# Kernel tuning notes

Measured on AMD Instinct MI355X. Metric: run time of the kernel, lower is better.

Reference implementation:

```python
import jax, jax.numpy as jnp
import numpy as np
from jax import lax

N, IN, OUT, R, K = 16384, 128, 128, 3, 16
H = IN  # DGL lstm aggregator: LSTM(in_feats, in_feats)


def setup_inputs() -> dict:
    key = jax.random.key(0)
    ks = jax.random.split(key, 10)
    s_in = np.float32(1.0 / np.sqrt(IN))
    return {
        "x": jax.random.normal(ks[0], (N, IN), jnp.float32),
        "conn": jax.random.normal(ks[1], (N, IN), jnp.float32),
        "nbr_idx": jax.random.randint(ks[2], (R, N, K), 0, N),
        "trans": jax.random.normal(ks[3], (OUT, IN), jnp.float32) * s_in,
        "W_ih": jax.random.normal(ks[4], (R, 4 * H, IN), jnp.float32) * s_in,
        "W_hh": jax.random.normal(ks[5], (R, 4 * H, H), jnp.float32) * s_in,
        "b_lstm": jnp.zeros((R, 4 * H), jnp.float32),
        "fc_self": jax.random.normal(ks[6], (R, OUT, IN), jnp.float32) * s_in,
        "fc_neigh": jax.random.normal(ks[7], (R, OUT, H), jnp.float32) * s_in,
        "bias": jnp.zeros((R, OUT), jnp.float32),
    }


def _lstm_last_hidden(seq, Wih, Whh, b):
    """seq: [N, K, IN] neighbor sequence -> final hidden state [N, H].
    PyTorch/DGL gate order: input, forget, cell, output."""
    n = seq.shape[0]
    h0 = jnp.zeros((n, H), seq.dtype)
    c0 = jnp.zeros((n, H), seq.dtype)

    def step(carry, x_t):
        h, c = carry
        gates = x_t @ Wih.T + h @ Whh.T + b  # [N, 4H]
        i, f, g, o = jnp.split(gates, 4, axis=-1)
        i = jax.nn.sigmoid(i)
        f = jax.nn.sigmoid(f)
        o = jax.nn.sigmoid(o)
        g = jnp.tanh(g)
        c = f * c + i * g
        h = o * jnp.tanh(c)
        return (h, c), None

    (h, _), _ = lax.scan(step, (h0, c0), jnp.swapaxes(seq, 0, 1))  # scan over K
    return h


def reference(x, conn, nbr_idx, trans, W_ih, W_hh, b_lstm, fc_self, fc_neigh, bias):
    outs = []
    for r in range(R):  # small fixed relation set
        nbr = x[nbr_idx[r]]  # [N, K, IN] irregular gather
        h_n = _lstm_last_hidden(nbr, W_ih[r], W_hh[r], b_lstm[r])
        o = x @ fc_self[r].T + h_n @ fc_neigh[r].T + bias[r]
        outs.append(jax.nn.leaky_relu(o))  # slope 0.01 == F.leaky_relu default
    X = jnp.stack(outs, axis=1)  # [N, R, OUT]
    # att_score = (X @ trans) @ conn[:, :, None], softmax over relations
    score = jnp.einsum('nrd,di,ni->nr', X, trans, conn)
    att = jax.nn.softmax(score, axis=1)
    return jnp.einsum('nrd,nr->nd', X, att)  # [N, OUT]
```

## Files before the change

kernel.cpp:

```cpp
#include <hip/hip_runtime.h>

#define NN    16384
#define HD    128
#define G4    512
#define KST   16
#define NRELS 3

using f16x8 = __attribute__((ext_vector_type(8))) _Float16;
using f32x4 = __attribute__((ext_vector_type(4))) float;

static __device__ __forceinline__ f32x4 f4splat(float v) {
    f32x4 r; r[0] = v; r[1] = v; r[2] = v; r[3] = v; return r;
}
static __device__ __forceinline__ f16x8 load8h(const float* p) {
    const float4 a = ((const float4*)p)[0];
    const float4 b = ((const float4*)p)[1];
    f16x8 r;
    r[0] = (_Float16)a.x; r[1] = (_Float16)a.y; r[2] = (_Float16)a.z; r[3] = (_Float16)a.w;
    r[4] = (_Float16)b.x; r[5] = (_Float16)b.y; r[6] = (_Float16)b.z; r[7] = (_Float16)b.w;
    return r;
}
static __device__ __forceinline__ f32x4 mfma16h(f16x8 a, f16x8 b, f32x4 c) {
    return __builtin_amdgcn_mfma_f32_16x16x32_f16(a, b, c, 0, 0, 0);
}
static __device__ __forceinline__ unsigned short f2h_bits(float f) {
    return __builtin_bit_cast(unsigned short, (_Float16)f);
}
static __device__ __forceinline__ float h2f(unsigned short b) {
    return (float)__builtin_bit_cast(_Float16, b);
}
static __device__ __forceinline__ float sigm(float x) {
    return __builtin_amdgcn_rcpf(1.0f + __expf(-x));
}
static __device__ __forceinline__ float tanh_(float x) {
    return 2.0f * __builtin_amdgcn_rcpf(1.0f + __expf(-2.0f * x)) - 1.0f;
}

template <int OUTC, int MODE>
__global__ __launch_bounds__(512, 2) void gemm_rt(
    const float* __restrict__ A, const float* __restrict__ W,
    const float* __restrict__ bias, void* __restrict__ outp)
{
    constexpr int CW = OUTC / 8;
    constexpr int CT = CW / 16;
    const int tid = threadIdx.x;
    const int w = tid >> 6, lane = tid & 63;
    const int g = lane >> 4, m = lane & 15;
    const int n0 = blockIdx.x * 64;
    const int r = blockIdx.y;
    const float* Wr = W + (size_t)r * OUTC * HD;

    f32x4 acc[4][CT];
#pragma unroll
    for (int rt = 0; rt < 4; ++rt)
#pragma unroll
        for (int ct = 0; ct < CT; ++ct) acc[rt][ct] = f4splat(0.0f);

#pragma unroll
    for (int kc = 0; kc < 4; ++kc) {
        f16x8 a[4];
#pragma unroll
        for (int rt = 0; rt < 4; ++rt)
            a[rt] = load8h(A + (size_t)(n0 + rt * 16 + m) * HD + kc * 32 + 8 * g);
        f16x8 b[CT];
#pragma unroll
        for (int ct = 0; ct < CT; ++ct)
            b[ct] = load8h(Wr + (size_t)(w * CW + ct * 16 + m) * HD + kc * 32 + 8 * g);
#pragma unroll
        for (int rt = 0; rt < 4; ++rt)
#pragma unroll
            for (int ct = 0; ct < CT; ++ct)
                acc[rt][ct] = mfma16h(a[rt], b[ct], acc[rt][ct]);
    }

#pragma unroll
    for (int rt = 0; rt < 4; ++rt)
#pragma unroll
        for (int ct = 0; ct < CT; ++ct) {
            const int col = w * CW + ct * 16 + m;
            const float bv = bias ? bias[r * OUTC + col] : 0.0f;
#pragma unroll
            for (int e = 0; e < 4; ++e) {
                const int row = n0 + rt * 16 + 4 * g + e;
                const float v = acc[rt][ct][e] + bv;
                if constexpr (MODE == 0) {
                    ((float*)outp)[(size_t)row * OUTC + col] = v;
                } else {
                    ((unsigned short*)outp)[((size_t)r * NN + row) * G4 + (size_t)(col & 127) * 4 + (col >> 7)] =
                        f2h_bits(v);
                }
            }
        }
}

__global__ __launch_bounds__(512, 2) void lstm_kernel(
    const float* __restrict__ x, const int* __restrict__ nbr,
    const float* __restrict__ Whh, const float* __restrict__ fcs,
    const float* __restrict__ fcn, const float* __restrict__ bias,
    const unsigned short* __restrict__ xW, float* __restrict__ Xout)
{
    __shared__ unsigned short h_lds[2][64 * HD];
    __shared__ int idx_lds[64 * KST];

    const int tid = threadIdx.x;
    const int w = tid >> 6, lane = tid & 63;
    const int g = lane >> 4, m = lane & 15;
    const int n0 = blockIdx.x * 64;
    const int r = blockIdx.y;

    for (int i = tid; i < 64 * KST; i += 512)
        idx_lds[i] = nbr[((size_t)r * NN + n0 + (i >> 4)) * KST + (i & 15)];

    f16x8 bw[4][4];
    const float* whr = Whh + (size_t)r * G4 * HD;
#pragma unroll
    for (int q = 0; q < 4; ++q)
#pragma unroll
        for (int kc = 0; kc < 4; ++kc)
            bw[q][kc] = load8h(whr + (size_t)(q * 128 + w * 16 + m) * HD + kc * 32 + 8 * g);

    float cst[4][4];
#pragma unroll
    for (int rt = 0; rt < 4; ++rt)
#pragma unroll
        for (int e = 0; e < 4; ++e) cst[rt][e] = 0.0f;

    const unsigned short* xwr = xW + (size_t)r * NN * G4;
    __syncthreads();

    ushort4 xv[4][4];
#pragma unroll
    for (int rt = 0; rt < 4; ++rt)
#pragma unroll
        for (int e = 0; e < 4; ++e) {
            const int nidx = idx_lds[(rt * 16 + 4 * g + e) * KST + 0];
            xv[rt][e] = *(const ushort4*)(xwr + (size_t)nidx * G4 + (size_t)(w * 16 + m) * 4);
        }

    int cur = 0;
    for (int t = 0; t < KST; ++t) {
        f32x4 acc[4][4];
#pragma unroll
        for (int rt = 0; rt < 4; ++rt)
#pragma unroll
            for (int e = 0; e < 4; ++e) {
                acc[rt][0][e] = h2f(xv[rt][e].x);
                acc[rt][1][e] = h2f(xv[rt][e].y);
                acc[rt][2][e] = h2f(xv[rt][e].z);
                acc[rt][3][e] = h2f(xv[rt][e].w);
            }

        if (t + 1 < KST) {
#pragma unroll
            for (int rt = 0; rt < 4; ++rt)
#pragma unroll
                for (int e = 0; e < 4; ++e) {
                    const int nidx = idx_lds[(rt * 16 + 4 * g + e) * KST + (t + 1)];
                    xv[rt][e] = *(const ushort4*)(xwr + (size_t)nidx * G4 + (size_t)(w * 16 + m) * 4);
                }
        }

        if (t > 0) {
            const unsigned short* hb = h_lds[cur];
#pragma unroll
            for (int kc = 0; kc < 4; ++kc) {
                f16x8 a[4];
#pragma unroll
                for (int rt = 0; rt < 4; ++rt) {
                    const int row = rt * 16 + m;
                    a[rt] = *(const f16x8*)&hb[row * HD + ((kc * 32 + 8 * g) ^ ((row & 7) << 3))];
                }
#pragma unroll
                for (int rt = 0; rt < 4; ++rt)
#pragma unroll
                    for (int q = 0; q < 4; ++q)
                        acc[rt][q] = mfma16h(a[rt], bw[q][kc], acc[rt][q]);
            }
        }

        unsigned short* nh = h_lds[cur ^ 1];
#pragma unroll
        for (int rt = 0; rt < 4; ++rt)
#pragma unroll
            for (int e = 0; e < 4; ++e) {
                const float iv = sigm(acc[rt][0][e]);
                const float fv = sigm(acc[rt][1][e]);
                const float gv = tanh_(acc[rt][2][e]);
                const float ov = sigm(acc[rt][3][e]);
                const float cn = fv * cst[rt][e] + iv * gv;
                cst[rt][e] = cn;
                const float hf = ov * tanh_(cn);
                const int row = rt * 16 + 4 * g + e;
                const int col = w * 16 + m;
                nh[row * HD + (col ^ ((row & 7) << 3))] = f2h_bits(hf);
            }
        __syncthreads();
        cur ^= 1;
    }

    {
        const int rt = w & 3;
        const int cth = (w >> 2) * 64;
        const float* fsr = fcs + (size_t)r * HD * HD;
        const float* fnr = fcn + (size_t)r * HD * HD;
        const unsigned short* hb = h_lds[cur];
        f32x4 oacc[4];
#pragma unroll
        for (int i = 0; i < 4; ++i)
            oacc[i] = f4splat(bias[r * HD + cth + i * 16 + m]);
#pragma unroll
        for (int kc = 0; kc < 4; ++kc) {
            const int row = rt * 16 + m;
            const f16x8 ax = load8h(x + (size_t)(n0 + row) * HD + kc * 32 + 8 * g);
            const f16x8 ah = *(const f16x8*)&hb[row * HD + ((kc * 32 + 8 * g) ^ ((row & 7) << 3))];
#pragma unroll
            for (int i = 0; i < 4; ++i) {
                const f16x8 bs = load8h(fsr + (size_t)(cth + i * 16 + m) * HD + kc * 32 + 8 * g);
                const f16x8 bn = load8h(fnr + (size_t)(cth + i * 16 + m) * HD + kc * 32 + 8 * g);
                oacc[i] = mfma16h(ax, bs, oacc[i]);
                oacc[i] = mfma16h(ah, bn, oacc[i]);
            }
        }
#pragma unroll
        for (int i = 0; i < 4; ++i)
#pragma unroll
            for (int e = 0; e < 4; ++e) {
                const int row = rt * 16 + 4 * g + e;
                const int col = cth + i * 16 + m;
                float v = oacc[i][e];
                v = v > 0.0f ? v : 0.01f * v;
                Xout[((size_t)(n0 + row) * NRELS + r) * HD + col] = v;
            }
    }
}

__global__ __launch_bounds__(256) void attn_kernel(
    const float* __restrict__ X, const float* __restrict__ tc,
    float* __restrict__ out)
{
    const int wv = blockIdx.x * (blockDim.x >> 6) + (threadIdx.x >> 6);
    const int lane = threadIdx.x & 63;
    if (wv >= NN) return;
    const size_t nb = (size_t)wv;

    const float t0 = tc[nb * HD + lane];
    const float t1 = tc[nb * HD + 64 + lane];
    float x0[3], x1[3], sc[3];
#pragma unroll
    for (int r = 0; r < 3; ++r) {
        x0[r] = X[(nb * 3 + r) * HD + lane];
        x1[r] = X[(nb * 3 + r) * HD + 64 + lane];
        float p = x0[r] * t0 + x1[r] * t1;
#pragma unroll
        for (int off = 32; off >= 1; off >>= 1)
            p += __shfl_xor(p, off, 64);
        sc[r] = p;
    }
    const float mx = fmaxf(sc[0], fmaxf(sc[1], sc[2]));
    const float e0 = __expf(sc[0] - mx), e1 = __expf(sc[1] - mx), e2 = __expf(sc[2] - mx);
    const float inv = __builtin_amdgcn_rcpf(e0 + e1 + e2);
    const float a0 = e0 * inv, a1 = e1 * inv, a2 = e2 * inv;
    out[nb * HD + lane]      = a0 * x0[0] + a1 * x0[1] + a2 * x0[2];
    out[nb * HD + 64 + lane] = a0 * x1[0] + a1 * x1[1] + a2 * x1[2];
}

extern "C" void kernel_launch(void* const* d_in, const int* in_sizes, int n_in,
                              void* d_out, int out_size, void* d_ws, size_t ws_size,
                              hipStream_t stream)
{
    const float* x     = (const float*)d_in[0];
    const float* conn  = (const float*)d_in[1];
    const int*   nbr   = (const int*)d_in[2];
    const float* trans = (const float*)d_in[3];
    const float* Wih   = (const float*)d_in[4];
    const float* Whh   = (const float*)d_in[5];
    const float* blstm = (const float*)d_in[6];
    const float* fcs   = (const float*)d_in[7];
    const float* fcn   = (const float*)d_in[8];
    const float* bias  = (const float*)d_in[9];
    float* out = (float*)d_out;

    const size_t XW_B = (size_t)NRELS * NN * G4 * 2;
    const size_t TC_B = (size_t)NN * HD * 4;
    const size_t XO_B = (size_t)NN * NRELS * HD * 4;
    if (ws_size < XW_B + TC_B + XO_B) return;

    char* wsb = (char*)d_ws;
    unsigned short* xW = (unsigned short*)wsb;
    float*          tc = (float*)(wsb + XW_B);
    float*          Xo = (float*)(wsb + XW_B + TC_B);

    gemm_rt<512, 1><<<dim3(NN / 64, NRELS), 512, 0, stream>>>(x, Wih, blstm, (void*)xW);
    gemm_rt<128, 0><<<dim3(NN / 64, 1), 512, 0, stream>>>(conn, trans, nullptr, (void*)tc);
    lstm_kernel<<<dim3(NN / 64, NRELS), 512, 0, stream>>>(x, nbr, Whh, fcs, fcn, bias, xW, Xo);
    attn_kernel<<<dim3(NN / 4), 256, 0, stream>>>(Xo, tc, out);
}
```

Baseline: 349.4 us.

## Split LSTM block into two half-tiles and interleave MFMA with gate math

Splits the 64-row tile of the recurrent LSTM loop into two independent 32-row halves (A and B), each with its own LDS hidden-state buffer and cell state. Each half-step runs the MFMA recurrence for one half while the other half does its sigmoid/tanh gate math, so matrix and transcendental work can overlap across the barrier. It also pre-scales neighbor indices into byte offsets in LDS so the gather address needs only one add. The cost is two barriers per timestep instead of one and more live registers, which matters under the 512-thread, 2-block launch bound.

```diff
diff --git a/kernel.cpp b/kernel.cpp
--- a/kernel.cpp
+++ b/kernel.cpp
@@ -93,13 +93,71 @@
         }
 }
 
+static __device__ __forceinline__ void consume_xw(f32x4 (&acc)[2][4], const ushort4 (&xv)[2][4]) {
+#pragma unroll
+    for (int rt = 0; rt < 2; ++rt)
+#pragma unroll
+        for (int e = 0; e < 4; ++e) {
+            acc[rt][0][e] = h2f(xv[rt][e].x);
+            acc[rt][1][e] = h2f(xv[rt][e].y);
+            acc[rt][2][e] = h2f(xv[rt][e].z);
+            acc[rt][3][e] = h2f(xv[rt][e].w);
+        }
+}
+static __device__ __forceinline__ void prefetch_xw(ushort4 (&xv)[2][4], const int* idxt, int t,
+                                                   const char* xwr, int laneoff, int g) {
+#pragma unroll
+    for (int rt = 0; rt < 2; ++rt)
+#pragma unroll
+        for (int e = 0; e < 4; ++e) {
+            const unsigned off = (unsigned)idxt[(rt * 16 + 4 * g + e) * KST + t] + laneoff;
+            xv[rt][e] = *(const ushort4*)(xwr + off);
+        }
+}
+static __device__ __forceinline__ void mfma_h(f32x4 (&acc)[2][4], const unsigned short* hbuf,
+                                              const f16x8 (&bw)[4][4], int m, int g) {
+#pragma unroll
+    for (int kc = 0; kc < 4; ++kc) {
+        f16x8 a[2];
+#pragma unroll
+        for (int rt = 0; rt < 2; ++rt) {
+            const int row = rt * 16 + m;
+            a[rt] = *(const f16x8*)&hbuf[row * HD + ((kc * 32 + 8 * g) ^ ((row & 7) << 3))];
+        }
+#pragma unroll
+        for (int rt = 0; rt < 2; ++rt)
+#pragma unroll
+            for (int q = 0; q < 4; ++q)
+                acc[rt][q] = mfma16h(a[rt], bw[q][kc], acc[rt][q]);
+    }
+}
+static __device__ __forceinline__ void lstm_elem(const f32x4 (&acc)[2][4], float (&cst)[2][4],
+                                                 unsigned short* hbuf, int g, int m, int w) {
+#pragma unroll
+    for (int rt = 0; rt < 2; ++rt)
+#pragma unroll
+        for (int e = 0; e < 4; ++e) {
+            const float iv = sigm(acc[rt][0][e]);
+            const float fv = sigm(acc[rt][1][e]);
+            const float gv = tanh_(acc[rt][2][e]);
+            const float ov = sigm(acc[rt][3][e]);
+            const float cn = fv * cst[rt][e] + iv * gv;
+            cst[rt][e] = cn;
+            const float hf = ov * tanh_(cn);
+            const int row = rt * 16 + 4 * g + e;
+            const int col = w * 16 + m;
+            hbuf[row * HD + (col ^ ((row & 7) << 3))] = f2h_bits(hf);
+        }
+}
+
 __global__ __launch_bounds__(512, 2) void lstm_kernel(
     const float* __restrict__ x, const int* __restrict__ nbr,
     const float* __restrict__ Whh, const float* __restrict__ fcs,
     const float* __restrict__ fcn, const float* __restrict__ bias,
     const unsigned short* __restrict__ xW, float* __restrict__ Xout)
 {
-    __shared__ unsigned short h_lds[2][64 * HD];
+    __shared__ unsigned short h_A[32 * HD];
+    __shared__ unsigned short h_B[32 * HD];
     __shared__ int idx_lds[64 * KST];
 
     const int tid = threadIdx.x;
@@ -107,9 +165,11 @@
     const int g = lane >> 4, m = lane & 15;
     const int n0 = blockIdx.x * 64;
     const int r = blockIdx.y;
+    const int laneoff = (w * 16 + m) * 8;
+    const char* xwr = (const char*)(xW + (size_t)r * NN * G4);
 
     for (int i = tid; i < 64 * KST; i += 512)
-        idx_lds[i] = nbr[((size_t)r * NN + n0 + (i >> 4)) * KST + (i & 15)];
+        idx_lds[i] = nbr[((size_t)r * NN + n0 + (i >> 4)) * KST + (i & 15)] << 10;
 
     f16x8 bw[4][4];
     const float* whr = Whh + (size_t)r * G4 * HD;
@@ -119,100 +179,50 @@
         for (int kc = 0; kc < 4; ++kc)
             bw[q][kc] = load8h(whr + (size_t)(q * 128 + w * 16 + m) * HD + kc * 32 + 8 * g);
 
-    float cst[4][4];
-#pragma unroll
-    for (int rt = 0; rt < 4; ++rt)
-#pragma unroll
-        for (int e = 0; e < 4; ++e) cst[rt][e] = 0.0f;
-
-    const unsigned short* xwr = xW + (size_t)r * NN * G4;
+    float cst_A[2][4], cst_B[2][4];
+#pragma unroll
+    for (int rt = 0; rt < 2; ++rt)
+#pragma unroll
+        for (int e = 0; e < 4; ++e) { cst_A[rt][e] = 0.0f; cst_B[rt][e] = 0.0f; }
+
     __syncthreads();
 
-    ushort4 xv[4][4];
-#pragma unroll
-    for (int rt = 0; rt < 4; ++rt)
-#pragma unroll
-        for (int e = 0; e < 4; ++e) {
-            const int nidx = idx_lds[(rt * 16 + 4 * g + e) * KST + 0];
-            xv[rt][e] = *(const ushort4*)(xwr + (size_t)nidx * G4 + (size_t)(w * 16 + m) * 4);
-        }
-
-    int cur = 0;
-    for (int t = 0; t < KST; ++t) {
-        f32x4 acc[4][4];
-#pragma unroll
-        for (int rt = 0; rt < 4; ++rt)
-#pragma unroll
-            for (int e = 0; e < 4; ++e) {
-                acc[rt][0][e] = h2f(xv[rt][e].x);
-                acc[rt][1][e] = h2f(xv[rt][e].y);
-                acc[rt][2][e] = h2f(xv[rt][e].z);
-                acc[rt][3][e] = h2f(xv[rt][e].w);
-            }
-
-        if (t + 1 < KST) {
-#pragma unroll
-            for (int rt = 0; rt < 4; ++rt)
-#pragma unroll
-                for (int e = 0; e < 4; ++e) {
-                    const int nidx = idx_lds[(rt * 16 + 4 * g + e) * KST + (t + 1)];
-                    xv[rt][e] = *(const ushort4*)(xwr + (size_t)nidx * G4 + (size_t)(w * 16 + m) * 4);
-                }
-        }
-
-        if (t > 0) {
-            const unsigned short* hb = h_lds[cur];
-#pragma unroll
-            for (int kc = 0; kc < 4; ++kc) {
-                f16x8 a[4];
-#pragma unroll
-                for (int rt = 0; rt < 4; ++rt) {
-                    const int row = rt * 16 + m;
-                    a[rt] = *(const f16x8*)&hb[row * HD + ((kc * 32 + 8 * g) ^ ((row & 7) << 3))];
-                }
-#pragma unroll
-                for (int rt = 0; rt < 4; ++rt)
-#pragma unroll
-                    for (int q = 0; q < 4; ++q)
-                        acc[rt][q] = mfma16h(a[rt], bw[q][kc], acc[rt][q]);
-            }
-        }
-
-        unsigned short* nh = h_lds[cur ^ 1];
-#pragma unroll
-        for (int rt = 0; rt < 4; ++rt)
-#pragma unroll
-            for (int e = 0; e < 4; ++e) {
-                const float iv = sigm(acc[rt][0][e]);
-                const float fv = sigm(acc[rt][1][e]);
-                const float gv = tanh_(acc[rt][2][e]);
-                const float ov = sigm(acc[rt][3][e]);
-                const float cn = fv * cst[rt][e] + iv * gv;
-                cst[rt][e] = cn;
-                const float hf = ov * tanh_(cn);
-                const int row = rt * 16 + 4 * g + e;
-                const int col = w * 16 + m;
-                nh[row * HD + (col ^ ((row & 7) << 3))] = f2h_bits(hf);
-            }
+    ushort4 xv_A[2][4], xv_B[2][4];
+    prefetch_xw(xv_A, idx_lds, 0, xwr, laneoff, g);
+    prefetch_xw(xv_B, idx_lds + 32 * KST, 0, xwr, laneoff, g);
+
+    f32x4 acc_A[2][4], acc_B[2][4];
+    for (int k = 0; k < KST; ++k) {
+        consume_xw(acc_A, xv_A);
+        if (k + 1 < KST) prefetch_xw(xv_A, idx_lds, k + 1, xwr, laneoff, g);
+        if (k > 0) mfma_h(acc_A, h_A, bw, m, g);
+        if (k > 0) lstm_elem(acc_B, cst_B, h_B, g, m, w);
         __syncthreads();
-        cur ^= 1;
-    }
+        consume_xw(acc_B, xv_B);
+        if (k + 1 < KST) prefetch_xw(xv_B, idx_lds + 32 * KST, k + 1, xwr, laneoff, g);
+        if (k > 0) mfma_h(acc_B, h_B, bw, m, g);
+        lstm_elem(acc_A, cst_A, h_A, g, m, w);
+        __syncthreads();
+    }
+    lstm_elem(acc_B, cst_B, h_B, g, m, w);
+    __syncthreads();
 
     {
-        const int rt = w & 3;
+        const int ert = w & 3;
         const int cth = (w >> 2) * 64;
+        const unsigned short* hb = (ert < 2) ? h_A : h_B;
+        const int lr0 = (ert & 1) * 16;
         const float* fsr = fcs + (size_t)r * HD * HD;
         const float* fnr = fcn + (size_t)r * HD * HD;
-        const unsigned short* hb = h_lds[cur];
         f32x4 oacc[4];
 #pragma unroll
         for (int i = 0; i < 4; ++i)
             oacc[i] = f4splat(bias[r * HD + cth + i * 16 + m]);
 #pragma unroll
         for (int kc = 0; kc < 4; ++kc) {
-            const int row = rt * 16 + m;
-            const f16x8 ax = load8h(x + (size_t)(n0 + row) * HD + kc * 32 + 8 * g);
-            const f16x8 ah = *(const f16x8*)&hb[row * HD + ((kc * 32 + 8 * g) ^ ((row & 7) << 3))];
+            const int lrow = lr0 + m;
+            const f16x8 ax = load8h(x + (size_t)(n0 + ert * 16 + m) * HD + kc * 32 + 8 * g);
+            const f16x8 ah = *(const f16x8*)&hb[lrow * HD + ((kc * 32 + 8 * g) ^ ((lrow & 7) << 3))];
 #pragma unroll
             for (int i = 0; i < 4; ++i) {
                 const f16x8 bs = load8h(fsr + (size_t)(cth + i * 16 + m) * HD + kc * 32 + 8 * g);
@@ -225,7 +235,7 @@
         for (int i = 0; i < 4; ++i)
 #pragma unroll
             for (int e = 0; e < 4; ++e) {
-                const int row = rt * 16 + 4 * g + e;
+                const int row = ert * 16 + 4 * g + e;
                 const int col = cth + i * 16 + m;
                 float v = oacc[i][e];
                 v = v > 0.0f ? v : 0.01f * v;
```

Result: faster. 335.2 us (-4.0%).

## Shrink LSTM block to 16 nodes to raise occupancy and cut registers

Applied to the files above, without the earlier changes.

The LSTM kernel now handles 16 nodes per block instead of 64. Each wave carries one row tile instead of four, which shrinks accumulator and prefetch register arrays, and launch bounds are raised to allow four blocks per CU. Neighbor indices are stored pre-shifted and transposed so one int4 LDS read serves four gathers, and the swizzled LDS offsets are precomputed. In exchange, the Whh fragments are reloaded by four times as many blocks, and each MFMA step has less independent work to hide latency.

```diff
diff --git a/kernel.cpp b/kernel.cpp
--- a/kernel.cpp
+++ b/kernel.cpp
@@ -5,6 +5,7 @@
 #define G4    512
 #define KST   16
 #define NRELS 3
+#define NPB   16
 
 using f16x8 = __attribute__((ext_vector_type(8))) _Float16;
 using f32x4 = __attribute__((ext_vector_type(4))) float;
@@ -93,23 +94,27 @@
         }
 }
 
-__global__ __launch_bounds__(512, 2) void lstm_kernel(
+__global__ __launch_bounds__(512, 4) void lstm_kernel(
     const float* __restrict__ x, const int* __restrict__ nbr,
     const float* __restrict__ Whh, const float* __restrict__ fcs,
     const float* __restrict__ fcn, const float* __restrict__ bias,
     const unsigned short* __restrict__ xW, float* __restrict__ Xout)
 {
-    __shared__ unsigned short h_lds[2][64 * HD];
-    __shared__ int idx_lds[64 * KST];
+    __shared__ unsigned short h_lds[2][NPB * HD];
+    __shared__ int idx_lds[KST * NPB];
 
     const int tid = threadIdx.x;
     const int w = tid >> 6, lane = tid & 63;
     const int g = lane >> 4, m = lane & 15;
-    const int n0 = blockIdx.x * 64;
+    const int n0 = blockIdx.x * NPB;
     const int r = blockIdx.y;
-
-    for (int i = tid; i < 64 * KST; i += 512)
-        idx_lds[i] = nbr[((size_t)r * NN + n0 + (i >> 4)) * KST + (i & 15)];
+    const unsigned laneoff = (unsigned)(w * 16 + m) * 8u;
+    const char* xwr = (const char*)(xW + (size_t)r * NN * G4);
+
+    if (tid < KST * NPB) {
+        const int t = tid >> 4, n = tid & 15;
+        idx_lds[tid] = nbr[((size_t)r * NN + n0 + n) * KST + t] << 10;
+    }
 
     f16x8 bw[4][4];
     const float* whr = Whh + (size_t)r * G4 * HD;
@@ -119,118 +124,95 @@
         for (int kc = 0; kc < 4; ++kc)
             bw[q][kc] = load8h(whr + (size_t)(q * 128 + w * 16 + m) * HD + kc * 32 + 8 * g);
 
-    float cst[4][4];
-#pragma unroll
-    for (int rt = 0; rt < 4; ++rt)
-#pragma unroll
-        for (int e = 0; e < 4; ++e) cst[rt][e] = 0.0f;
-
-    const unsigned short* xwr = xW + (size_t)r * NN * G4;
+    int rd_off[4], wr_off[4];
+#pragma unroll
+    for (int kc = 0; kc < 4; ++kc)
+        rd_off[kc] = m * HD + ((kc * 32 + 8 * g) ^ ((m & 7) << 3));
+#pragma unroll
+    for (int e = 0; e < 4; ++e) {
+        const int row = 4 * g + e;
+        wr_off[e] = row * HD + ((w * 16 + m) ^ ((row & 7) << 3));
+    }
+
+    float cst[4] = {0.0f, 0.0f, 0.0f, 0.0f};
     __syncthreads();
 
-    ushort4 xv[4][4];
-#pragma unroll
-    for (int rt = 0; rt < 4; ++rt)
-#pragma unroll
-        for (int e = 0; e < 4; ++e) {
-            const int nidx = idx_lds[(rt * 16 + 4 * g + e) * KST + 0];
-            xv[rt][e] = *(const ushort4*)(xwr + (size_t)nidx * G4 + (size_t)(w * 16 + m) * 4);
-        }
+    ushort4 xv[4];
+    {
+        const int4 i4 = *(const int4*)&idx_lds[4 * g];
+        xv[0] = *(const ushort4*)(xwr + (unsigned)i4.x + laneoff);
+        xv[1] = *(const ushort4*)(xwr + (unsigned)i4.y + laneoff);
+        xv[2] = *(const ushort4*)(xwr + (unsigned)i4.z + laneoff);
+        xv[3] = *(const ushort4*)(xwr + (unsigned)i4.w + laneoff);
+    }
 
     int cur = 0;
     for (int t = 0; t < KST; ++t) {
-        f32x4 acc[4][4];
-#pragma unroll
-        for (int rt = 0; rt < 4; ++rt)
-#pragma unroll
-            for (int e = 0; e < 4; ++e) {
-                acc[rt][0][e] = h2f(xv[rt][e].x);
-                acc[rt][1][e] = h2f(xv[rt][e].y);
-                acc[rt][2][e] = h2f(xv[rt][e].z);
-                acc[rt][3][e] = h2f(xv[rt][e].w);
-            }
+        f32x4 acc[4];
+#pragma unroll
+        for (int e = 0; e < 4; ++e) {
+            acc[0][e] = h2f(xv[e].x);
+            acc[1][e] = h2f(xv[e].y);
+            acc[2][e] = h2f(xv[e].z);
+            acc[3][e] = h2f(xv[e].w);
+        }
 
         if (t + 1 < KST) {
-#pragma unroll
-            for (int rt = 0; rt < 4; ++rt)
-#pragma unroll
-                for (int e = 0; e < 4; ++e) {
-                    const int nidx = idx_lds[(rt * 16 + 4 * g + e) * KST + (t + 1)];
-                    xv[rt][e] = *(const ushort4*)(xwr + (size_t)nidx * G4 + (size_t)(w * 16 + m) * 4);
-                }
+            const int4 i4 = *(const int4*)&idx_lds[(t + 1) * 16 + 4 * g];
+            xv[0] = *(const ushort4*)(xwr + (unsigned)i4.x + laneoff);
+            xv[1] = *(const ushort4*)(xwr + (unsigned)i4.y + laneoff);
+            xv[2] = *(const ushort4*)(xwr + (unsigned)i4.z + laneoff);
+            xv[3] = *(const ushort4*)(xwr + (unsigned)i4.w + laneoff);
         }
 
         if (t > 0) {
             const unsigned short* hb = h_lds[cur];
 #pragma unroll
             for (int kc = 0; kc < 4; ++kc) {
-                f16x8 a[4];
-#pragma unroll
-                for (int rt = 0; rt < 4; ++rt) {
-                    const int row = rt * 16 + m;
-                    a[rt] = *(const f16x8*)&hb[row * HD + ((kc * 32 + 8 * g) ^ ((row & 7) << 3))];
-                }
-#pragma unroll
-                for (int rt = 0; rt < 4; ++rt)
-#pragma unroll
-                    for (int q = 0; q < 4; ++q)
-                        acc[rt][q] = mfma16h(a[rt], bw[q][kc], acc[rt][q]);
+                const f16x8 a = *(const f16x8*)&hb[rd_off[kc]];
+#pragma unroll
+                for (int q = 0; q < 4; ++q)
+                    acc[q] = mfma16h(a, bw[q][kc], acc[q]);
             }
         }
 
         unsigned short* nh = h_lds[cur ^ 1];
 #pragma unroll
-        for (int rt = 0; rt < 4; ++rt)
-#pragma unroll
-            for (int e = 0; e < 4; ++e) {
-                const float iv = sigm(acc[rt][0][e]);
-                const float fv = sigm(acc[rt][1][e]);
-                const float gv = tanh_(acc[rt][2][e]);
-                const float ov = sigm(acc[rt][3][e]);
-                const float cn = fv * cst[rt][e] + iv * gv;
-                cst[rt][e] = cn;
-                const float hf = ov * tanh_(cn);
-                const int row = rt * 16 + 4 * g + e;
-                const int col = w * 16 + m;
-                nh[row * HD + (col ^ ((row & 7) << 3))] = f2h_bits(hf);
-            }
+        for (int e = 0; e < 4; ++e) {
+            const float iv = sigm(acc[0][e]);
+            const float fv = sigm(acc[1][e]);
+            const float gv = tanh_(acc[2][e]);
+            const float ov = sigm(acc[3][e]);
+            const float cn = fv * cst[e] + iv * gv;
+            cst[e] = cn;
+            nh[wr_off[e]] = f2h_bits(ov * tanh_(cn));
+        }
         __syncthreads();
         cur ^= 1;
     }
 
     {
-        const int rt = w & 3;
-        const int cth = (w >> 2) * 64;
+        const unsigned short* hb = h_lds[cur];
         const float* fsr = fcs + (size_t)r * HD * HD;
         const float* fnr = fcn + (size_t)r * HD * HD;
-        const unsigned short* hb = h_lds[cur];
-        f32x4 oacc[4];
-#pragma unroll
-        for (int i = 0; i < 4; ++i)
-            oacc[i] = f4splat(bias[r * HD + cth + i * 16 + m]);
+        const int col = w * 16 + m;
+        f32x4 oacc = f4splat(bias[r * HD + col]);
 #pragma unroll
         for (int kc = 0; kc < 4; ++kc) {
-            const int row = rt * 16 + m;
-            const f16x8 ax = load8h(x + (size_t)(n0 + row) * HD + kc * 32 + 8 * g);
-            const f16x8 ah = *(const f16x8*)&hb[row * HD + ((kc * 32 + 8 * g) ^ ((row & 7) << 3))];
-#pragma unroll
-            for (int i = 0; i < 4; ++i) {
-                const f16x8 bs = load8h(fsr + (size_t)(cth + i * 16 + m) * HD + kc * 32 + 8 * g);
-                const f16x8 bn = load8h(fnr + (size_t)(cth + i * 16 + m) * HD + kc * 32 + 8 * g);
-                oacc[i] = mfma16h(ax, bs, oacc[i]);
-                oacc[i] = mfma16h(ah, bn, oacc[i]);
-            }
-        }
-#pragma unroll
-        for (int i = 0; i < 4; ++i)
-#pragma unroll
-            for (int e = 0; e < 4; ++e) {
-                const int row = rt * 16 + 4 * g + e;
-                const int col = cth + i * 16 + m;
-                float v = oacc[i][e];
-                v = v > 0.0f ? v : 0.01f * v;
-                Xout[((size_t)(n0 + row) * NRELS + r) * HD + col] = v;
-            }
+            const f16x8 ax = load8h(x + (size_t)(n0 + m) * HD + kc * 32 + 8 * g);
+            const f16x8 ah = *(const f16x8*)&hb[rd_off[kc]];
+            const f16x8 bs = load8h(fsr + (size_t)col * HD + kc * 32 + 8 * g);
+            const f16x8 bn = load8h(fnr + (size_t)col * HD + kc * 32 + 8 * g);
+            oacc = mfma16h(ax, bs, oacc);
+            oacc = mfma16h(ah, bn, oacc);
+        }
+#pragma unroll
+        for (int e = 0; e < 4; ++e) {
+            const int row = 4 * g + e;
+            float v = oacc[e];
+            v = v > 0.0f ? v : 0.01f * v;
+            Xout[((size_t)(n0 + row) * NRELS + r) * HD + col] = v;
+        }
     }
 }
 
@@ -292,6 +274,6 @@
 
     gemm_rt<512, 1><<<dim3(NN / 64, NRELS), 512, 0, stream>>>(x, Wih, blstm, (void*)xW);
     gemm_rt<128, 0><<<dim3(NN / 64, 1), 512, 0, stream>>>(conn, trans, nullptr, (void*)tc);
-    lstm_kernel<<<dim3(NN / 64, NRELS), 512, 0, stream>>>(x, nbr, Whh, fcs, fcn, bias, xW, Xo);
+    lstm_kernel<<<dim3(NN / NPB, NRELS), 512, 0, stream>>>(x, nbr, Whh, fcs, fcn, bias, xW, Xo);
     attn_kernel<<<dim3(NN / 4), 256, 0, stream>>>(Xo, tc, out);
 }
```

New measurement: 334.4 us. 4.3% less time.
